# Kernel tuning notes

Measured on AMD Instinct MI355X. Metric: run time of the kernel, lower is better.

## Reference

```python
import jax, jax.numpy as jnp
import numpy as np

B, N, DIM, H, DH = 4, 2048, 512, 8, 64
INNER = H * DH  # 512
SCALE = DH ** -0.5


def setup_inputs() -> dict:
    key = jax.random.key(0)
    k1, k2, k3, k4 = jax.random.split(key, 4)
    x = jax.random.normal(k1, (B, N, DIM), dtype=jnp.float32)
    bias = jax.random.normal(k2, (B, N, DIM), dtype=jnp.float32)
    # to_qkv: Linear(dim, inner*3, bias=False)
    w_qkv = jax.random.normal(k3, (DIM, 3 * INNER), dtype=jnp.float32) * (DIM ** -0.5)
    # to_out: Linear(inner, dim) with bias (project_out=True since heads != 1)
    w_out = jax.random.normal(k4, (INNER, DIM), dtype=jnp.float32) * (INNER ** -0.5)
    b_out = jnp.zeros((DIM,), dtype=jnp.float32)
    return {"x": x, "bias": bias, "w_qkv": w_qkv, "w_out": w_out, "b_out": b_out}


def _split_heads(t):
    # [b, n, h*d] -> [b, h, n, d]
    b, n, _ = t.shape
    return t.reshape(b, n, H, DH).transpose(0, 2, 1, 3)


def reference(x, bias, w_qkv, w_out, b_out):
    qkv = x @ w_qkv  # [b, n, 3*inner]
    q, k, v = jnp.split(qkv, 3, axis=-1)
    q, k, v = map(_split_heads, (q, k, v))
    dots = jnp.einsum('bhid,bhjd->bhij', q, k) * SCALE  # [b,h,n,n]

    qkv_b = bias @ w_qkv
    qb, kb, _ = jnp.split(qkv_b, 3, axis=-1)
    qb, kb = _split_heads(qb), _split_heads(kb)
    dots = dots + jnp.einsum('bhid,bhjd->bhij', qb, kb) * SCALE

    attn = jax.nn.softmax(dots, axis=-1)
    out = jnp.einsum('bhij,bhjd->bhid', attn, v)  # [b,h,n,d]
    out = out.transpose(0, 2, 1, 3).reshape(x.shape[0], x.shape[1], INNER)
    return out @ w_out + b_out
```

## Files before the change

### kernel.cpp

```cpp
#include <hip/hip_runtime.h>
#include <hip/hip_bf16.h>

#define DEV __device__ __forceinline__

typedef __attribute__((ext_vector_type(8))) short short8;
typedef __attribute__((ext_vector_type(4))) int i32x4;
typedef __attribute__((ext_vector_type(2))) int i32x2;
typedef __attribute__((ext_vector_type(4))) float f32x4;
typedef __attribute__((ext_vector_type(16))) float f32x16;

constexpr int B = 4, N = 2048, H = 8, DH = 64;
constexpr int INNER = H * DH;
constexpr int BH = B * H;
constexpr float QSCALE = 0.125f * 1.44269504088896f;

constexpr size_t OFF_WQKVT = 0;
constexpr size_t OFF_WOUTT = OFF_WQKVT + (size_t)1536 * 512;
constexpr size_t OFF_QT    = OFF_WOUTT + (size_t)512 * 512;
constexpr size_t OFF_KT    = OFF_QT + (size_t)BH * N * 128;
constexpr size_t OFF_VT    = OFF_KT + (size_t)BH * N * 128;
constexpr size_t OFF_AO    = OFF_VT + (size_t)BH * DH * N;
constexpr size_t OFF_XBF   = OFF_AO + (size_t)8192 * 512;
constexpr size_t OFF_BBF   = OFF_AO;

DEV short f2b(float f) {
    __hip_bfloat16 h = __float2bfloat16(f);
    return __builtin_bit_cast(short, h);
}

DEV int cvtpk(float lo, float hi) {
    int r;
    asm("v_cvt_pk_bf16_f32 %0, %1, %2" : "=v"(r) : "v"(lo), "v"(hi));
    return r;
}

DEV float fexp2(float x) {
    float r;
    asm("v_exp_f32 %0, %1" : "=v"(r) : "v"(x));
    return r;
}

DEV void plswap(int& a, int& b) {
    i32x2 r = __builtin_amdgcn_permlane32_swap(a, b, false, false);
    a = r.x; b = r.y;
}

DEV void gload16(const void* g, void* l) {
    __builtin_amdgcn_global_load_lds(
        (const __attribute__((address_space(1))) unsigned int*)g,
        (__attribute__((address_space(3))) unsigned int*)l, 16, 0, 0);
}

__global__ void prep_kernel(const float* __restrict__ wqkv,
                            const float* __restrict__ wout,
                            const float* __restrict__ x,
                            const float* __restrict__ bias,
                            __hip_bfloat16* __restrict__ ws) {
    __hip_bfloat16* wqkvT = ws + OFF_WQKVT;
    __hip_bfloat16* woutT = ws + OFF_WOUTT;
    short8* xbf = (short8*)(ws + OFF_XBF);
    short8* bbf = (short8*)(ws + OFF_BBF);
    int tid = blockIdx.x * blockDim.x + threadIdx.x;
    const int nconv = 8192 * 512 / 8;
    const int t1 = 512 * 1536 / 4;
    const int t2 = 512 * 512 / 4;
    const int total = 2 * nconv + t1 + t2;
    for (int i = tid; i < total; i += gridDim.x * blockDim.x) {
        if (i < 2 * nconv) {
            const float4* src = (const float4*)(i < nconv ? x : bias);
            short8* dst = i < nconv ? xbf : bbf;
            int j = i < nconv ? i : i - nconv;
            float4 v0 = src[2 * j], v1 = src[2 * j + 1];
            short8 sv;
            sv[0] = f2b(v0.x); sv[1] = f2b(v0.y); sv[2] = f2b(v0.z); sv[3] = f2b(v0.w);
            sv[4] = f2b(v1.x); sv[5] = f2b(v1.y); sv[6] = f2b(v1.z); sv[7] = f2b(v1.w);
            dst[j] = sv;
        } else if (i < 2 * nconv + t1) {
            int j = i - 2 * nconv;
            int k  = j / 384;
            int c4 = (j % 384) * 4;
            float4 v = ((const float4*)wqkv)[j];
            wqkvT[(size_t)(c4 + 0) * 512 + k] = __float2bfloat16(v.x);
            wqkvT[(size_t)(c4 + 1) * 512 + k] = __float2bfloat16(v.y);
            wqkvT[(size_t)(c4 + 2) * 512 + k] = __float2bfloat16(v.z);
            wqkvT[(size_t)(c4 + 3) * 512 + k] = __float2bfloat16(v.w);
        } else {
            int j = i - 2 * nconv - t1;
            int k  = j / 128;
            int c4 = (j % 128) * 4;
            float4 v = ((const float4*)wout)[j];
            woutT[(size_t)(c4 + 0) * 512 + k] = __float2bfloat16(v.x);
            woutT[(size_t)(c4 + 1) * 512 + k] = __float2bfloat16(v.y);
            woutT[(size_t)(c4 + 2) * 512 + k] = __float2bfloat16(v.z);
            woutT[(size_t)(c4 + 3) * 512 + k] = __float2bfloat16(v.w);
        }
    }
}

__global__ __launch_bounds__(256) void gemm_qkv(__hip_bfloat16* __restrict__ ws) {
    int mt = blockIdx.x, yt = blockIdx.y;
    bool src_is_bias = (yt >= 12);
    int nt = src_is_bias ? yt - 12 : yt;
    const short* A  = (const short*)(ws + (src_is_bias ? OFF_BBF : OFF_XBF));
    const short* Bt = (const short*)(ws + OFF_WQKVT);
    int m0 = mt * 128, n0 = nt * 128;
    bool isV = (!src_is_bias && nt >= 8);

    __shared__ __align__(16) short As[128][64];
    __shared__ __align__(16) short Bs[128][64];

    int tid  = threadIdx.x;
    int wave = tid >> 6, lane = tid & 63;
    int wrow = wave >> 1, wcol = wave & 1;
    int lg = lane >> 4, li = lane & 15;

    f32x4 acc[4][4] = {};

    auto kloop = [&](bool swp) {
        for (int k0 = 0; k0 < 512; k0 += 64) {
#pragma unroll
            for (int i = 0; i < 4; ++i) {
                int c = wave * 4 + i;
                int r = c * 8 + (lane >> 3);
                gload16((const char*)A + ((size_t)(m0 + r) * 512 + k0 + (lane & 7) * 8) * 2,
                        (char*)&As[0][0] + c * 1024);
                gload16((const char*)Bt + ((size_t)(n0 + r) * 512 + k0 + (lane & 7) * 8) * 2,
                        (char*)&Bs[0][0] + c * 1024);
            }
            __syncthreads();
#pragma unroll
            for (int ks = 0; ks < 2; ++ks) {
                short8 af[4], bf[4];
#pragma unroll
                for (int m = 0; m < 4; ++m)
                    af[m] = *(const short8*)(&As[wrow * 64 + m * 16 + li][ks * 32 + lg * 8]);
#pragma unroll
                for (int n = 0; n < 4; ++n)
                    bf[n] = *(const short8*)(&Bs[wcol * 64 + n * 16 + li][ks * 32 + lg * 8]);
#pragma unroll
                for (int m = 0; m < 4; ++m)
#pragma unroll
                    for (int n = 0; n < 4; ++n)
                        acc[m][n] = swp
                            ? __builtin_amdgcn_mfma_f32_16x16x32_bf16(bf[n], af[m], acc[m][n], 0, 0, 0)
                            : __builtin_amdgcn_mfma_f32_16x16x32_bf16(af[m], bf[n], acc[m][n], 0, 0, 0);
            }
            __syncthreads();
        }
    };
    if (isV) kloop(false); else kloop(true);

    __hip_bfloat16* QT = ws + OFF_QT;
    __hip_bfloat16* KT = ws + OFF_KT;
    __hip_bfloat16* VT = ws + OFF_VT;

    if (isV) {
        int cc_base = n0 - 1024 + wcol * 64;
#pragma unroll
        for (int m = 0; m < 4; ++m) {
            int row0 = m0 + wrow * 64 + m * 16 + lg * 4;
            int b = row0 >> 11, nn = row0 & 2047;
#pragma unroll
            for (int n = 0; n < 4; ++n) {
                int cc = cc_base + n * 16 + li;
                int h = cc >> 6, d = cc & 63;
                int w0 = cvtpk(acc[m][n][0], acc[m][n][1]);
                int w1 = cvtpk(acc[m][n][2], acc[m][n][3]);
                short* p = (short*)VT + (size_t)((b * H + h) * DH + d) * N + nn;
                i32x2 wv = { w0, w1 };
                *(i32x2*)p = wv;
            }
        }
    } else {
        int qkoff = src_is_bias ? 64 : 0;
        bool isQ = (n0 < 512);
#pragma unroll
        for (int m = 0; m < 4; ++m) {
            int row = m0 + wrow * 64 + m * 16 + li;
            int b = row >> 11, nn = row & 2047;
#pragma unroll
            for (int n = 0; n < 4; ++n) {
                int cc0 = n0 + wcol * 64 + n * 16 + lg * 4;
                int w0, w1;
                short* p;
                if (isQ) {
                    int h = cc0 >> 6, d0 = (cc0 & 63) + qkoff;
                    w0 = cvtpk(acc[m][n][0] * QSCALE, acc[m][n][1] * QSCALE);
                    w1 = cvtpk(acc[m][n][2] * QSCALE, acc[m][n][3] * QSCALE);
                    p = (short*)QT + ((size_t)(b * H + h) * N + nn) * 128 + d0;
                } else {
                    int c = cc0 - 512;
                    int h = c >> 6, d0 = (c & 63) + qkoff;
                    w0 = cvtpk(acc[m][n][0], acc[m][n][1]);
                    w1 = cvtpk(acc[m][n][2], acc[m][n][3]);
                    p = (short*)KT + ((size_t)(b * H + h) * N + nn) * 128 + d0;
                }
                i32x2 wv = { w0, w1 };
                *(i32x2*)p = wv;
            }
        }
    }
}

__global__ __launch_bounds__(256, 2) void attn_kernel(__hip_bfloat16* __restrict__ ws) {
    int bid = blockIdx.x;
    int c   = bid & 7;
    int idx = bid >> 3;
    int bh  = (idx & 3) * 8 + c;
    int qb  = idx >> 2;

    int wave = threadIdx.x >> 6, lane = threadIdx.x & 63;
    int li32 = lane & 31, hi = lane >> 5;
    int qr0 = qb * 128 + wave * 32;

    const short* QT  = (const short*)(ws + OFF_QT) + (size_t)bh * N * 128;
    const char*  KTg = (const char*)((const short*)(ws + OFF_KT) + (size_t)bh * N * 128);
    const char*  VTg = (const char*)((const short*)(ws + OFF_VT) + (size_t)bh * DH * N);

    __shared__ __align__(16) short Ktile[3][64][128];
    __shared__ __align__(16) short Vtile[3][64][64];

    short8 qf[8];
#pragma unroll
    for (int kc = 0; kc < 8; ++kc)
        qf[kc] = *(const short8*)(QT + (size_t)(qr0 + li32) * 128 + kc * 16 + hi * 8);

    float m_run = -3e38f, l_run = 0.f;
    f32x16 o[2] = {};

    auto stage = [&](int t, int bsel) {
        int kv0 = t * 64;
        char* Kd = (char*)&Ktile[0][0][0] + bsel * 16384;
        char* Vd = (char*)&Vtile[0][0][0] + bsel * 8192;
#pragma unroll
        for (int cc = 0; cc < 4; ++cc) {
            int ck = wave * 4 + cc;
            int r  = ck * 4 + (lane >> 4);
            int cbx = (lane & 15) * 16;
            gload16(KTg + (size_t)(kv0 + r) * 256 + (cbx ^ ((r & 7) << 4)), Kd + ck * 1024);
        }
#pragma unroll
        for (int cc = 0; cc < 2; ++cc) {
            int ck = wave * 2 + cc;
            int r  = ck * 8 + (lane >> 3);
            int cbx = (lane & 7) * 16;
            gload16(VTg + (size_t)r * 4096 + kv0 * 2 + (cbx ^ ((r & 7) << 4)), Vd + ck * 1024);
        }
    };

    auto tile = [&](int bsel) {
        const char* Kb = (const char*)&Ktile[0][0][0] + bsel * 16384;
        const char* Vb = (const char*)&Vtile[0][0][0] + bsel * 8192;

        f32x16 sT[2] = {};
        __builtin_amdgcn_s_setprio(1);
#pragma unroll
        for (int sub = 0; sub < 2; ++sub) {
            int row = sub * 32 + li32;
            int sw  = (row & 7) << 4;
            const char* kbase = Kb + row * 256;
#pragma unroll
            for (int kc = 0; kc < 8; ++kc) {
                short8 kf = *(const short8*)(kbase + ((kc * 32 + hi * 16) ^ sw));
                sT[sub] = __builtin_amdgcn_mfma_f32_32x32x16_bf16(kf, qf[kc], sT[sub], 0, 0, 0);
            }
        }
        __builtin_amdgcn_s_setprio(0);

        float t0[8];
#pragma unroll
        for (int j = 0; j < 8; ++j)
            t0[j] = fmaxf(fmaxf(sT[0][j], sT[0][j + 8]), fmaxf(sT[1][j], sT[1][j + 8]));
        float pm = fmaxf(fmaxf(fmaxf(t0[0], t0[1]), fmaxf(t0[2], t0[3])),
                         fmaxf(fmaxf(t0[4], t0[5]), fmaxf(t0[6], t0[7])));
        pm = fmaxf(pm, __shfl_xor(pm, 32));

        if (__any(pm > m_run + 8.f)) {
            float mn = fmaxf(m_run, pm);
            float al = fexp2(m_run - mn);
#pragma unroll
            for (int a = 0; a < 2; ++a)
#pragma unroll
                for (int r = 0; r < 16; ++r) o[a][r] *= al;
            l_run *= al;
            m_run = mn;
        }

        float lsp[4] = {0.f, 0.f, 0.f, 0.f};
        int w[2][8];
#pragma unroll
        for (int sub = 0; sub < 2; ++sub)
#pragma unroll
            for (int r2 = 0; r2 < 8; ++r2) {
                float p0 = fexp2(sT[sub][2 * r2]     - m_run);
                float p1 = fexp2(sT[sub][2 * r2 + 1] - m_run);
                lsp[r2 & 3] += p0 + p1;
                w[sub][r2] = cvtpk(p0, p1);
            }
        l_run += (lsp[0] + lsp[1]) + (lsp[2] + lsp[3]);

        short8 pf[2][2];
#pragma unroll
        for (int sub = 0; sub < 2; ++sub) {
            plswap(w[sub][0], w[sub][2]); plswap(w[sub][1], w[sub][3]);
            plswap(w[sub][4], w[sub][6]); plswap(w[sub][5], w[sub][7]);
            i32x4 f0 = { w[sub][0], w[sub][1], w[sub][2], w[sub][3] };
            i32x4 f1 = { w[sub][4], w[sub][5], w[sub][6], w[sub][7] };
            pf[sub][0] = __builtin_bit_cast(short8, f0);
            pf[sub][1] = __builtin_bit_cast(short8, f1);
        }

        __builtin_amdgcn_s_setprio(1);
#pragma unroll
        for (int sub = 0; sub < 2; ++sub)
#pragma unroll
            for (int ksel = 0; ksel < 2; ++ksel) {
                int cc = sub * 2 + ksel;
#pragma unroll
                for (int a = 0; a < 2; ++a) {
                    int row = a * 32 + li32;
                    int sw  = (row & 7) << 4;
                    short8 vf = *(const short8*)(Vb + row * 128 + ((cc * 32 + hi * 16) ^ sw));
                    o[a] = __builtin_amdgcn_mfma_f32_32x32x16_bf16(vf, pf[sub][ksel], o[a], 0, 0, 0);
                }
            }
        __builtin_amdgcn_s_setprio(0);
    };

    stage(0, 0);
    stage(1, 1);

    int bsel = 0;
    for (int t = 0; t < 32; ++t) {
        if (t < 31) asm volatile("s_waitcnt vmcnt(6)" ::: "memory");
        else        asm volatile("s_waitcnt vmcnt(0)" ::: "memory");
        __builtin_amdgcn_s_barrier();
        __builtin_amdgcn_sched_barrier(0);
        if (t + 2 < 32) {
            int b2 = bsel + 2 >= 3 ? bsel - 1 : bsel + 2;
            stage(t + 2, b2);
        }
        tile(bsel);
        bsel = bsel + 1 >= 3 ? 0 : bsel + 1;
    }

    l_run += __shfl_xor(l_run, 32);
    __hip_bfloat16* AO = ws + OFF_AO;
    int b = bh >> 3, h = bh & 7;
    char* tb = (char*)&Ktile[0][0][0] + wave * 4096;
    float inv = 1.f / l_run;
#pragma unroll
    for (int a = 0; a < 2; ++a)
#pragma unroll
        for (int r2 = 0; r2 < 8; ++r2) {
            int r = 2 * r2;
            int dv = (r & 3) + 8 * (r >> 2) + 4 * hi + 32 * a;
            int word = cvtpk(o[a][r] * inv, o[a][r + 1] * inv);
            *(int*)(tb + li32 * 128 + ((dv * 2) ^ ((li32 & 7) << 4))) = word;
        }
#pragma unroll
    for (int qq = 0; qq < 32; qq += 8) {
        int q = qq + (lane >> 3), seg = lane & 7;
        short8 vrow = *(const short8*)(tb + q * 128 + ((seg * 16) ^ ((q & 7) << 4)));
        *(short8*)(AO + (size_t)(b * N + qr0 + q) * INNER + h * 64 + seg * 8) = vrow;
    }
}

__global__ __launch_bounds__(256) void gemm_out(const __hip_bfloat16* __restrict__ ws_c,
                                                const float* __restrict__ bout,
                                                float* __restrict__ out) {
    const short* AO = (const short*)(ws_c + OFF_AO);
    const short* Bt = (const short*)(ws_c + OFF_WOUTT);
    int m0 = blockIdx.x * 128, n0 = blockIdx.y * 128;

    __shared__ __align__(16) short As[128][64];
    __shared__ __align__(16) short Bs[128][64];

    int tid  = threadIdx.x;
    int wave = tid >> 6, lane = tid & 63;
    int wrow = wave >> 1, wcol = wave & 1;
    int lg = lane >> 4, li = lane & 15;

    f32x4 acc[4][4] = {};

    for (int k0 = 0; k0 < 512; k0 += 64) {
#pragma unroll
        for (int i = 0; i < 4; ++i) {
            int c = wave * 4 + i;
            int r = c * 8 + (lane >> 3);
            gload16((const char*)AO + ((size_t)(m0 + r) * 512 + k0 + (lane & 7) * 8) * 2,
                    (char*)&As[0][0] + c * 1024);
            gload16((const char*)Bt + ((size_t)(n0 + r) * 512 + k0 + (lane & 7) * 8) * 2,
                    (char*)&Bs[0][0] + c * 1024);
        }
        __syncthreads();
#pragma unroll
        for (int ks = 0; ks < 2; ++ks) {
            short8 af[4], bf[4];
#pragma unroll
            for (int m = 0; m < 4; ++m)
                af[m] = *(const short8*)(&As[wrow * 64 + m * 16 + li][ks * 32 + lg * 8]);
#pragma unroll
            for (int n = 0; n < 4; ++n)
                bf[n] = *(const short8*)(&Bs[wcol * 64 + n * 16 + li][ks * 32 + lg * 8]);
#pragma unroll
            for (int m = 0; m < 4; ++m)
#pragma unroll
                for (int n = 0; n < 4; ++n)
                    acc[m][n] = __builtin_amdgcn_mfma_f32_16x16x32_bf16(bf[n], af[m], acc[m][n], 0, 0, 0);
        }
        __syncthreads();
    }

    float4 bb[4];
#pragma unroll
    for (int n = 0; n < 4; ++n)
        bb[n] = *(const float4*)(bout + n0 + wcol * 64 + n * 16 + lg * 4);
#pragma unroll
    for (int m = 0; m < 4; ++m) {
        int row = m0 + wrow * 64 + m * 16 + li;
#pragma unroll
        for (int n = 0; n < 4; ++n) {
            int c0 = n0 + wcol * 64 + n * 16 + lg * 4;
            float4 v = { acc[m][n][0] + bb[n].x, acc[m][n][1] + bb[n].y,
                         acc[m][n][2] + bb[n].z, acc[m][n][3] + bb[n].w };
            *(float4*)(out + (size_t)row * 512 + c0) = v;
        }
    }
}

extern "C" void kernel_launch(void* const* d_in, const int* in_sizes, int n_in,
                              void* d_out, int out_size, void* d_ws, size_t ws_size,
                              hipStream_t stream) {
    const float* x    = (const float*)d_in[0];
    const float* bias = (const float*)d_in[1];
    const float* wqkv = (const float*)d_in[2];
    const float* wout = (const float*)d_in[3];
    const float* bout = (const float*)d_in[4];
    float* out = (float*)d_out;
    __hip_bfloat16* ws = (__hip_bfloat16*)d_ws;

    hipLaunchKernelGGL(prep_kernel, dim3(2048), dim3(256), 0, stream, wqkv, wout, x, bias, ws);
    hipLaunchKernelGGL(gemm_qkv, dim3(64, 20), dim3(256), 0, stream, ws);
    hipLaunchKernelGGL(attn_kernel, dim3(512), dim3(256), 0, stream, ws);
    hipLaunchKernelGGL(gemm_out, dim3(64, 4), dim3(256), 0, stream, (const __hip_bfloat16*)ws, bout, out);
}
```

Before: 140.8 us.

## Process two 32-row query blocks per wave in attention to reuse K/V tiles

Each wave of the attention kernel now handles 64 query rows (two 32-row halves) instead of 32, so every K and V fragment read from LDS feeds two MFMAs. The block covers 256 query rows and the grid is halved from 512 to 256 blocks. Launch bounds drop to one block per SM to allow roughly double the registers for the extra accumulators. This cuts LDS reads and global K/V staging per query, but 256 blocks may leave the 256 CUs at lower occupancy with less latency hiding.

New measurement: 162.3 us. 1.15x slower.

```diff
diff --git a/kernel.cpp b/kernel.cpp
--- a/kernel.cpp
+++ b/kernel.cpp
@@ -202,7 +202,7 @@
     }
 }
 
-__global__ __launch_bounds__(256, 2) void attn_kernel(__hip_bfloat16* __restrict__ ws) {
+__global__ __launch_bounds__(256, 1) void attn_kernel(__hip_bfloat16* __restrict__ ws) {
     int bid = blockIdx.x;
     int c   = bid & 7;
     int idx = bid >> 3;
@@ -211,7 +211,7 @@
 
     int wave = threadIdx.x >> 6, lane = threadIdx.x & 63;
     int li32 = lane & 31, hi = lane >> 5;
-    int qr0 = qb * 128 + wave * 32;
+    int qr0 = qb * 256 + wave * 64;
 
     const short* QT  = (const short*)(ws + OFF_QT) + (size_t)bh * N * 128;
     const char*  KTg = (const char*)((const short*)(ws + OFF_KT) + (size_t)bh * N * 128);
@@ -220,13 +220,16 @@
     __shared__ __align__(16) short Ktile[3][64][128];
     __shared__ __align__(16) short Vtile[3][64][64];
 
-    short8 qf[8];
-#pragma unroll
-    for (int kc = 0; kc < 8; ++kc)
-        qf[kc] = *(const short8*)(QT + (size_t)(qr0 + li32) * 128 + kc * 16 + hi * 8);
-
-    float m_run = -3e38f, l_run = 0.f;
-    f32x16 o[2] = {};
+    short8 qf0[8], qf1[8];
+#pragma unroll
+    for (int kc = 0; kc < 8; ++kc) {
+        qf0[kc] = *(const short8*)(QT + (size_t)(qr0 + li32) * 128 + kc * 16 + hi * 8);
+        qf1[kc] = *(const short8*)(QT + (size_t)(qr0 + 32 + li32) * 128 + kc * 16 + hi * 8);
+    }
+
+    const f32x16 Z16 = {};
+    float m0 = -3e38f, l0 = 0.f, m1 = -3e38f, l1 = 0.f;
+    f32x16 o0[2] = {}, o1[2] = {};
 
     auto stage = [&](int t, int bsel) {
         int kv0 = t * 64;
@@ -248,25 +251,8 @@
         }
     };
 
-    auto tile = [&](int bsel) {
-        const char* Kb = (const char*)&Ktile[0][0][0] + bsel * 16384;
-        const char* Vb = (const char*)&Vtile[0][0][0] + bsel * 8192;
-
-        f32x16 sT[2] = {};
-        __builtin_amdgcn_s_setprio(1);
-#pragma unroll
-        for (int sub = 0; sub < 2; ++sub) {
-            int row = sub * 32 + li32;
-            int sw  = (row & 7) << 4;
-            const char* kbase = Kb + row * 256;
-#pragma unroll
-            for (int kc = 0; kc < 8; ++kc) {
-                short8 kf = *(const short8*)(kbase + ((kc * 32 + hi * 16) ^ sw));
-                sT[sub] = __builtin_amdgcn_mfma_f32_32x32x16_bf16(kf, qf[kc], sT[sub], 0, 0, 0);
-            }
-        }
-        __builtin_amdgcn_s_setprio(0);
-
+    auto softmax_half = [&](f32x16 (&sT)[2], float& m_run, float& l_run,
+                            f32x16 (&o)[2], short8 (&pf)[2][2]) {
         float t0[8];
 #pragma unroll
         for (int j = 0; j < 8; ++j)
@@ -299,7 +285,6 @@
             }
         l_run += (lsp[0] + lsp[1]) + (lsp[2] + lsp[3]);
 
-        short8 pf[2][2];
 #pragma unroll
         for (int sub = 0; sub < 2; ++sub) {
             plswap(w[sub][0], w[sub][2]); plswap(w[sub][1], w[sub][3]);
@@ -309,6 +294,36 @@
             pf[sub][0] = __builtin_bit_cast(short8, f0);
             pf[sub][1] = __builtin_bit_cast(short8, f1);
         }
+    };
+
+    auto tile = [&](int bsel) {
+        const char* Kb = (const char*)&Ktile[0][0][0] + bsel * 16384;
+        const char* Vb = (const char*)&Vtile[0][0][0] + bsel * 8192;
+
+        f32x16 s0[2], s1[2];
+        __builtin_amdgcn_s_setprio(1);
+#pragma unroll
+        for (int sub = 0; sub < 2; ++sub) {
+            int row = sub * 32 + li32;
+            int sw  = (row & 7) << 4;
+            const char* kbase = Kb + row * 256;
+            {
+                short8 kf = *(const short8*)(kbase + ((hi * 16) ^ sw));
+                s0[sub] = __builtin_amdgcn_mfma_f32_32x32x16_bf16(kf, qf0[0], Z16, 0, 0, 0);
+                s1[sub] = __builtin_amdgcn_mfma_f32_32x32x16_bf16(kf, qf1[0], Z16, 0, 0, 0);
+            }
+#pragma unroll
+            for (int kc = 1; kc < 8; ++kc) {
+                short8 kf = *(const short8*)(kbase + ((kc * 32 + hi * 16) ^ sw));
+                s0[sub] = __builtin_amdgcn_mfma_f32_32x32x16_bf16(kf, qf0[kc], s0[sub], 0, 0, 0);
+                s1[sub] = __builtin_amdgcn_mfma_f32_32x32x16_bf16(kf, qf1[kc], s1[sub], 0, 0, 0);
+            }
+        }
+        __builtin_amdgcn_s_setprio(0);
+
+        short8 pf0[2][2], pf1[2][2];
+        softmax_half(s0, m0, l0, o0, pf0);
+        softmax_half(s1, m1, l1, o1, pf1);
 
         __builtin_amdgcn_s_setprio(1);
 #pragma unroll
@@ -321,7 +336,8 @@
                     int row = a * 32 + li32;
                     int sw  = (row & 7) << 4;
                     short8 vf = *(const short8*)(Vb + row * 128 + ((cc * 32 + hi * 16) ^ sw));
-                    o[a] = __builtin_amdgcn_mfma_f32_32x32x16_bf16(vf, pf[sub][ksel], o[a], 0, 0, 0);
+                    o0[a] = __builtin_amdgcn_mfma_f32_32x32x16_bf16(vf, pf0[sub][ksel], o0[a], 0, 0, 0);
+                    o1[a] = __builtin_amdgcn_mfma_f32_32x32x16_bf16(vf, pf1[sub][ksel], o1[a], 0, 0, 0);
                 }
             }
         __builtin_amdgcn_s_setprio(0);
@@ -344,22 +360,27 @@
         bsel = bsel + 1 >= 3 ? 0 : bsel + 1;
     }
 
-    l_run += __shfl_xor(l_run, 32);
+    __syncthreads();
+
+    l0 += __shfl_xor(l0, 32);
+    l1 += __shfl_xor(l1, 32);
     __hip_bfloat16* AO = ws + OFF_AO;
     int b = bh >> 3, h = bh & 7;
-    char* tb = (char*)&Ktile[0][0][0] + wave * 4096;
-    float inv = 1.f / l_run;
+    char* tb = (char*)&Ktile[0][0][0] + wave * 8192;
+    float inv0 = 1.f / l0, inv1 = 1.f / l1;
 #pragma unroll
     for (int a = 0; a < 2; ++a)
 #pragma unroll
         for (int r2 = 0; r2 < 8; ++r2) {
             int r = 2 * r2;
             int dv = (r & 3) + 8 * (r >> 2) + 4 * hi + 32 * a;
-            int word = cvtpk(o[a][r] * inv, o[a][r + 1] * inv);
-            *(int*)(tb + li32 * 128 + ((dv * 2) ^ ((li32 & 7) << 4))) = word;
-        }
-#pragma unroll
-    for (int qq = 0; qq < 32; qq += 8) {
+            int w0 = cvtpk(o0[a][r] * inv0, o0[a][r + 1] * inv0);
+            int w1 = cvtpk(o1[a][r] * inv1, o1[a][r + 1] * inv1);
+            *(int*)(tb + li32 * 128 + ((dv * 2) ^ ((li32 & 7) << 4))) = w0;
+            *(int*)(tb + (32 + li32) * 128 + ((dv * 2) ^ ((li32 & 7) << 4))) = w1;
+        }
+#pragma unroll
+    for (int qq = 0; qq < 64; qq += 8) {
         int q = qq + (lane >> 3), seg = lane & 7;
         short8 vrow = *(const short8*)(tb + q * 128 + ((seg * 16) ^ ((q & 7) << 4)));
         *(short8*)(AO + (size_t)(b * N + qr0 + q) * INNER + h * 64 + seg * 8) = vrow;
@@ -442,6 +463,6 @@
 
     hipLaunchKernelGGL(prep_kernel, dim3(2048), dim3(256), 0, stream, wqkv, wout, x, bias, ws);
     hipLaunchKernelGGL(gemm_qkv, dim3(64, 20), dim3(256), 0, stream, ws);
-    hipLaunchKernelGGL(attn_kernel, dim3(512), dim3(256), 0, stream, ws);
+    hipLaunchKernelGGL(attn_kernel, dim3(256), dim3(256), 0, stream, ws);
     hipLaunchKernelGGL(gemm_out, dim3(64, 4), dim3(256), 0, stream, (const __hip_bfloat16*)ws, bout, out);
 }
```
